# Kernel tuning notes

Measured on AMD Instinct MI355X. Metric: run time of the kernel, lower is better.

## Reference

```python
import jax, jax.numpy as jnp
import numpy as np

N_NODES = 32768
AGENTS = 32            # agents per sample (fully connected)
N_SAMPLES = N_NODES // AGENTS
N_EDGES = N_SAMPLES * AGENTS * (AGENTS - 1)  # 1,015,808
D = 64                 # latent_size
EDGE_DIM = 2
Z_DIM = 2 * D + EDGE_DIM  # CGConv concat width = 130
BN_EPS = 1e-5


def _build_block_edge_index():
    # fully-connected (no self-loop) blocks of AGENTS nodes, offset per sample
    a = np.arange(AGENTS)
    src, dst = np.meshgrid(a, a, indexing='ij')
    mask = src != dst
    src, dst = src[mask], dst[mask]              # [AGENTS*(AGENTS-1)]
    offs = (np.arange(N_SAMPLES) * AGENTS)[:, None]
    src = (src[None, :] + offs).reshape(-1)
    dst = (dst[None, :] + offs).reshape(-1)
    return jnp.asarray(np.stack([src, dst]), dtype=jnp.int64)


def setup_inputs() -> dict:
    key = jax.random.key(0)
    ks = jax.random.split(key, 16)
    x = jax.random.normal(ks[0], (N_NODES, D), dtype=jnp.float32)
    edge_index = _build_block_edge_index()                      # [2, E]
    edge_attr = jax.random.normal(ks[1], (N_EDGES, EDGE_DIM), dtype=jnp.float32)
    s = 1.0 / np.sqrt(Z_DIM)
    params = {}
    for li, base in ((1, 2), (2, 8)):
        params[f'Wf{li}'] = jax.random.uniform(ks[base + 0], (Z_DIM, D), jnp.float32, -s, s)
        params[f'bf{li}'] = jax.random.uniform(ks[base + 1], (D,), jnp.float32, -s, s)
        params[f'Ws{li}'] = jax.random.uniform(ks[base + 2], (Z_DIM, D), jnp.float32, -s, s)
        params[f'bs{li}'] = jax.random.uniform(ks[base + 3], (D,), jnp.float32, -s, s)
        params[f'gamma{li}'] = jnp.ones((D,), jnp.float32)
        params[f'beta{li}'] = jnp.zeros((D,), jnp.float32)
    return {'x': x, 'edge_index': edge_index, 'edge_attr': edge_attr, **params}


def _cgconv(x, edge_index, edge_attr, Wf, bf, Ws, bs, gamma, beta):
    src, dst = edge_index[0], edge_index[1]
    # z_ij = [x_i, x_j, e_ij], i = target (dst), j = source (src)
    z = jnp.concatenate([x[dst], x[src], edge_attr], axis=-1)       # [E, Z_DIM]
    m = jax.nn.sigmoid(z @ Wf + bf) * jax.nn.softplus(z @ Ws + bs)  # gated message
    agg = jax.ops.segment_sum(m, dst, num_segments=x.shape[0])      # scatter-add
    mu = jnp.mean(agg, axis=0)
    var = jnp.var(agg, axis=0)
    agg = (agg - mu) * jax.lax.rsqrt(var + BN_EPS) * gamma + beta   # train-mode BN
    return agg + x                                                  # residual


def reference(x, edge_index, edge_attr,
              Wf1, bf1, Ws1, bs1, gamma1, beta1,
              Wf2, bf2, Ws2, bs2, gamma2, beta2):
    h = jax.nn.relu(_cgconv(x, edge_index, edge_attr, Wf1, bf1, Ws1, bs1, gamma1, beta1))
    out = jax.nn.relu(_cgconv(h, edge_index, edge_attr, Wf2, bf2, Ws2, bs2, gamma2, beta2))
    return out
```

## Files before the change

kernel.cpp:

```cpp
#include <hip/hip_runtime.h>


#define NSAMP 1024
#define AG 32
#define DD 64
#define EPB 992
#define NN 32768
#define R1S 132

typedef float f4 __attribute__((ext_vector_type(4)));
typedef float f2 __attribute__((ext_vector_type(2)));

#define L2E 1.44269504088896340736f
#define BN_EPS_SCALED (1e-5 * (double)L2E * (double)L2E)

__device__ __forceinline__ void gacc(f4& acc, const f4 mf, const f4 ms) {
#pragma unroll
  for (int k = 0; k < 4; ++k) {
    float sig = __builtin_amdgcn_rcpf(1.0f + __builtin_amdgcn_exp2f(-mf[k]));
    float sp  = fmaxf(ms[k], 0.0f)
              + __builtin_amdgcn_logf(1.0f + __builtin_amdgcn_exp2f(-fabsf(ms[k])));
    acc[k] += sig * sp;
  }
}

template <int SRC>
__device__ __forceinline__ void gpass(const float* __restrict__ Wf,
                                      const float* __restrict__ bfv,
                                      const float* __restrict__ Ws,
                                      const float* __restrict__ bsv,
                                      const float* xb, float* R1,
                                      int t, int rbase) {
  const int tx = t & 31, ty = t >> 5;
  const int q = tx >> 4;
  const int cc0 = (tx & 15) * 4;
  const float* wbase = (q ? Ws : Wf) + SRC * (64 * 64) + cc0;
  constexpr int RPT = (SRC == 0) ? 2 : 4;
  f4 acc[RPT];
  if constexpr (SRC == 0) {
    const float* bv = q ? bsv : bfv;
    f4 b = *(const f4*)(bv + cc0);
#pragma unroll
    for (int r = 0; r < RPT; ++r) acc[r] = b;
  } else {
    f4 z = {0.f, 0.f, 0.f, 0.f};
#pragma unroll
    for (int r = 0; r < RPT; ++r) acc[r] = z;
  }
#pragma unroll 4
  for (int k4 = 0; k4 < 16; ++k4) {
    const float* wp = wbase + k4 * 256;
    f4 w0 = *(const f4*)(wp);
    f4 w1 = *(const f4*)(wp + 64);
    f4 w2 = *(const f4*)(wp + 128);
    f4 w3 = *(const f4*)(wp + 192);
#pragma unroll
    for (int r = 0; r < RPT; ++r) {
      const int row = (SRC == 0) ? (rbase + ty * RPT + r) : (ty * RPT + r);
      f4 xv = *(const f4*)&xb[row * 64 + k4 * 4];
      acc[r] += xv.x * w0 + xv.y * w1 + xv.z * w2 + xv.w * w3;
    }
  }
#pragma unroll
  for (int r = 0; r < RPT; ++r)
    *(f4*)&R1[(ty * RPT + r) * R1S + q * 64 + cc0] = acc[r] * L2E;
}

__device__ __forceinline__ void layer_body(
    int t, int s, int rbase, const float* __restrict__ ea,
    const float* __restrict__ Wf, const float* __restrict__ bfv,
    const float* __restrict__ Ws, const float* __restrict__ bsv,
    float* xb, float* R1, float* __restrict__ agg, double* __restrict__ stats)
{
  gpass<0>(Wf, bfv, Ws, bsv, xb, R1, t, rbase);
  __syncthreads();
  const int il = t >> 4, c0 = (t & 15) * 4;
  f4 af  = *(const f4*)&R1[il * R1S + c0];
  f4 as_ = *(const f4*)&R1[il * R1S + 64 + c0];
  __syncthreads();
  gpass<1>(Wf, bfv, Ws, bsv, xb, R1, t, 0);

  f4 wf0 = *(const f4*)(Wf + 128 * 64 + c0) * L2E;
  f4 wf1 = *(const f4*)(Wf + 129 * 64 + c0) * L2E;
  f4 ws0 = *(const f4*)(Ws + 128 * 64 + c0) * L2E;
  f4 ws1 = *(const f4*)(Ws + 129 * 64 + c0) * L2E;
  __syncthreads();

  {
    const f2* esrc = ((const f2*)ea) + (size_t)s * EPB;
    f2* ed = (f2*)xb;
    for (int u = t; u < EPB; u += 256) ed[u] = esrc[u];
  }
  __syncthreads();

  const int i = rbase + il;
  f4 acc = {0.f, 0.f, 0.f, 0.f};
  for (int jj = 0; jj < 31; ++jj) {
    const int ge = (jj >= i) ? 1 : 0;
    const int j  = jj + ge;
    const int e  = j * 31 + i - 1 + ge;
    f2 eav = *(const f2*)&xb[e * 2];
    f4 bf_ = *(const f4*)&R1[j * R1S + c0];
    f4 bs_ = *(const f4*)&R1[j * R1S + 64 + c0];
    f4 mf = af  + bf_ + eav.x * wf0 + eav.y * wf1;
    f4 ms = as_ + bs_ + eav.x * ws0 + eav.y * ws1;
    gacc(acc, mf, ms);
  }
  *(f4*)(agg + ((size_t)s * AG + i) * DD + c0) = acc;

  f4 s1 = acc, sq = acc * acc;
#pragma unroll
  for (int k = 0; k < 4; ++k) {
    s1[k] += __shfl_xor(s1[k], 16); sq[k] += __shfl_xor(sq[k], 16);
    s1[k] += __shfl_xor(s1[k], 32); sq[k] += __shfl_xor(sq[k], 32);
  }
  __syncthreads();
  if (t < 128) R1[t] = 0.0f;
  __syncthreads();
  if ((t & 63) < 16) {
#pragma unroll
    for (int k = 0; k < 4; ++k) {
      atomicAdd(&R1[c0 + k],      s1[k]);
      atomicAdd(&R1[64 + c0 + k], sq[k]);
    }
  }
  __syncthreads();
  if (t < 128) atomicAdd(&stats[t], (double)R1[t]);
}

__global__ __launch_bounds__(256, 4) void k_edge1(
    const float* __restrict__ x, const float* __restrict__ ea,
    const float* __restrict__ Wf, const float* __restrict__ bfv,
    const float* __restrict__ Ws, const float* __restrict__ bsv,
    float* __restrict__ agg, double* __restrict__ stats)
{
  __shared__ __align__(16) float xb[2048];
  __shared__ __align__(16) float R1[32 * R1S];
  const int t = threadIdx.x, b = blockIdx.x;
  const int s = b >> 1, rbase = (b & 1) * 16;
  {
    const f4* src = (const f4*)(x + (size_t)s * AG * DD);
    f4* dst = (f4*)xb;
    dst[t]       = src[t];
    dst[t + 256] = src[t + 256];
  }
  __syncthreads();
  layer_body(t, s, rbase, ea, Wf, bfv, Ws, bsv, xb, R1, agg, stats);
}

__global__ __launch_bounds__(256, 4) void k_edge2(
    const float* __restrict__ x, const float* __restrict__ ea,
    const float* __restrict__ Wf, const float* __restrict__ bfv,
    const float* __restrict__ Ws, const float* __restrict__ bsv,
    const double* __restrict__ stats1, const float* __restrict__ gmv,
    const float* __restrict__ btv, float* __restrict__ hout,
    const float* __restrict__ agg1, float* __restrict__ agg2,
    double* __restrict__ stats2)
{
  __shared__ __align__(16) float xb[2048];
  __shared__ __align__(16) float R1[32 * R1S];
  const int t = threadIdx.x, b = blockIdx.x;
  const int s = b >> 1, rbase = (b & 1) * 16;

  if (t < 64) {
    double mu  = stats1[t] * (1.0 / NN);
    double var = stats1[64 + t] * (1.0 / NN) - mu * mu;
    float rs = (float)(1.0 / sqrt(var + BN_EPS_SCALED));
    float g  = gmv[t] * rs;
    R1[t]      = g;
    R1[64 + t] = btv[t] - (float)mu * g;
  }
  __syncthreads();
  {
    const int row = t >> 3, cc = (t & 7) * 8;
    const size_t base = ((size_t)s * AG + row) * DD + cc;
    f4 sc0 = *(const f4*)&R1[cc],      sc1 = *(const f4*)&R1[cc + 4];
    f4 sh0 = *(const f4*)&R1[64 + cc], sh1 = *(const f4*)&R1[64 + cc + 4];
    f4 a0 = *(const f4*)(agg1 + base), a1 = *(const f4*)(agg1 + base + 4);
    f4 x0 = *(const f4*)(x + base),    x1 = *(const f4*)(x + base + 4);
    f4 h0 = a0 * sc0 + sh0 + x0;
    f4 h1 = a1 * sc1 + sh1 + x1;
#pragma unroll
    for (int k = 0; k < 4; ++k) { h0[k] = fmaxf(h0[k], 0.f); h1[k] = fmaxf(h1[k], 0.f); }
    *(f4*)(hout + base)     = h0;
    *(f4*)(hout + base + 4) = h1;
    *(f4*)&xb[row * DD + cc]     = h0;
    *(f4*)&xb[row * DD + cc + 4] = h1;
  }
  __syncthreads();
  layer_body(t, s, rbase, ea, Wf, bfv, Ws, bsv, xb, R1, agg2, stats2);
}

__global__ __launch_bounds__(256) void k_norm(
    const float* __restrict__ agg, const double* __restrict__ stats,
    const float* __restrict__ gmv, const float* __restrict__ btv,
    float* __restrict__ outp)
{
  __shared__ __align__(16) float sc[DD];
  __shared__ __align__(16) float sh[DD];
  const int t = threadIdx.x;
  if (t < DD) {
    double mu  = stats[t] * (1.0 / NN);
    double var = stats[DD + t] * (1.0 / NN) - mu * mu;
    float rs = (float)(1.0 / sqrt(var + BN_EPS_SCALED));
    float g  = gmv[t] * rs;
    sc[t] = g;
    sh[t] = btv[t] - (float)mu * g;
  }
  __syncthreads();
  const int idx = blockIdx.x * 256 + t;
  const int c   = (idx * 4) & (DD - 1);
  f4 a = ((const f4*)agg)[idx];
  f4 h = ((const f4*)outp)[idx];
  f4 r = a * (*(const f4*)&sc[c]) + (*(const f4*)&sh[c]) + h;
#pragma unroll
  for (int k = 0; k < 4; ++k) r[k] = fmaxf(r[k], 0.0f);
  ((f4*)outp)[idx] = r;
}

extern "C" void kernel_launch(void* const* d_in, const int* in_sizes, int n_in,
                              void* d_out, int out_size, void* d_ws, size_t ws_size,
                              hipStream_t stream) {
  const float* x   = (const float*)d_in[0];
  const float* ea  = (const float*)d_in[2];
  const float* Wf1 = (const float*)d_in[3];
  const float* bf1 = (const float*)d_in[4];
  const float* Ws1 = (const float*)d_in[5];
  const float* bs1 = (const float*)d_in[6];
  const float* gm1 = (const float*)d_in[7];
  const float* bt1 = (const float*)d_in[8];
  const float* Wf2 = (const float*)d_in[9];
  const float* bf2 = (const float*)d_in[10];
  const float* Ws2 = (const float*)d_in[11];
  const float* bs2 = (const float*)d_in[12];
  const float* gm2 = (const float*)d_in[13];
  const float* bt2 = (const float*)d_in[14];

  double* stats = (double*)d_ws;
  float*  agg1  = (float*)((char*)d_ws + 4096);
  float*  agg2  = (float*)((char*)d_ws + 4096 + (size_t)NN * DD * 4);
  float*  outp  = (float*)d_out;

  hipMemsetAsync(d_ws, 0, 2048, stream);
  k_edge1<<<2 * NSAMP, 256, 0, stream>>>(x, ea, Wf1, bf1, Ws1, bs1, agg1, stats);
  k_edge2<<<2 * NSAMP, 256, 0, stream>>>(x, ea, Wf2, bf2, Ws2, bs2,
                                         stats, gm1, bt1, outp, agg1, agg2,
                                         stats + 128);
  k_norm<<<NN * DD / 4 / 256, 256, 0, stream>>>(agg2, stats + 128, gm2, bt2, outp);
}
```

Before: 294.6 us.

## Process each sample in one 512-thread block to drop duplicated source projection

Each sample's 32 nodes are now handled by a single 512-thread block instead of two 256-thread blocks of 16 target rows each. Before, each half-block recomputed the full 32-row source-side projection, so that GEMM ran twice per sample; now it runs once. The two aggregation buffers are merged into one, with layer 2 reading its own sample's rows before overwriting them. The risk is that launch_bounds(512,4) lowers the per-thread register budget, which could cause spilling, and there are half as many blocks to spread across the GPU.

```diff
diff --git a/kernel.cpp b/kernel.cpp
--- a/kernel.cpp
+++ b/kernel.cpp
@@ -29,24 +29,21 @@
                                       const float* __restrict__ bfv,
                                       const float* __restrict__ Ws,
                                       const float* __restrict__ bsv,
-                                      const float* xb, float* R1,
-                                      int t, int rbase) {
+                                      const float* xb, float* R1, int t) {
   const int tx = t & 31, ty = t >> 5;
   const int q = tx >> 4;
   const int cc0 = (tx & 15) * 4;
   const float* wbase = (q ? Ws : Wf) + SRC * (64 * 64) + cc0;
-  constexpr int RPT = (SRC == 0) ? 2 : 4;
-  f4 acc[RPT];
+  f4 acc0, acc1;
   if constexpr (SRC == 0) {
     const float* bv = q ? bsv : bfv;
     f4 b = *(const f4*)(bv + cc0);
-#pragma unroll
-    for (int r = 0; r < RPT; ++r) acc[r] = b;
+    acc0 = b; acc1 = b;
   } else {
     f4 z = {0.f, 0.f, 0.f, 0.f};
-#pragma unroll
-    for (int r = 0; r < RPT; ++r) acc[r] = z;
-  }
+    acc0 = z; acc1 = z;
+  }
+  const int r0 = ty * 2;
 #pragma unroll 4
   for (int k4 = 0; k4 < 16; ++k4) {
     const float* wp = wbase + k4 * 256;
@@ -54,31 +51,28 @@
     f4 w1 = *(const f4*)(wp + 64);
     f4 w2 = *(const f4*)(wp + 128);
     f4 w3 = *(const f4*)(wp + 192);
-#pragma unroll
-    for (int r = 0; r < RPT; ++r) {
-      const int row = (SRC == 0) ? (rbase + ty * RPT + r) : (ty * RPT + r);
-      f4 xv = *(const f4*)&xb[row * 64 + k4 * 4];
-      acc[r] += xv.x * w0 + xv.y * w1 + xv.z * w2 + xv.w * w3;
-    }
-  }
-#pragma unroll
-  for (int r = 0; r < RPT; ++r)
-    *(f4*)&R1[(ty * RPT + r) * R1S + q * 64 + cc0] = acc[r] * L2E;
+    f4 xv0 = *(const f4*)&xb[r0 * 64 + k4 * 4];
+    f4 xv1 = *(const f4*)&xb[(r0 + 1) * 64 + k4 * 4];
+    acc0 += xv0.x * w0 + xv0.y * w1 + xv0.z * w2 + xv0.w * w3;
+    acc1 += xv1.x * w0 + xv1.y * w1 + xv1.z * w2 + xv1.w * w3;
+  }
+  *(f4*)&R1[r0 * R1S + q * 64 + cc0]       = acc0 * L2E;
+  *(f4*)&R1[(r0 + 1) * R1S + q * 64 + cc0] = acc1 * L2E;
 }
 
 __device__ __forceinline__ void layer_body(
-    int t, int s, int rbase, const float* __restrict__ ea,
+    int t, int s, const float* __restrict__ ea,
     const float* __restrict__ Wf, const float* __restrict__ bfv,
     const float* __restrict__ Ws, const float* __restrict__ bsv,
     float* xb, float* R1, float* __restrict__ agg, double* __restrict__ stats)
 {
-  gpass<0>(Wf, bfv, Ws, bsv, xb, R1, t, rbase);
-  __syncthreads();
-  const int il = t >> 4, c0 = (t & 15) * 4;
-  f4 af  = *(const f4*)&R1[il * R1S + c0];
-  f4 as_ = *(const f4*)&R1[il * R1S + 64 + c0];
-  __syncthreads();
-  gpass<1>(Wf, bfv, Ws, bsv, xb, R1, t, 0);
+  gpass<0>(Wf, bfv, Ws, bsv, xb, R1, t);
+  __syncthreads();
+  const int i = t >> 4, c0 = (t & 15) * 4;
+  f4 af  = *(const f4*)&R1[i * R1S + c0];
+  f4 as_ = *(const f4*)&R1[i * R1S + 64 + c0];
+  __syncthreads();
+  gpass<1>(Wf, bfv, Ws, bsv, xb, R1, t);
 
   f4 wf0 = *(const f4*)(Wf + 128 * 64 + c0) * L2E;
   f4 wf1 = *(const f4*)(Wf + 129 * 64 + c0) * L2E;
@@ -89,11 +83,10 @@
   {
     const f2* esrc = ((const f2*)ea) + (size_t)s * EPB;
     f2* ed = (f2*)xb;
-    for (int u = t; u < EPB; u += 256) ed[u] = esrc[u];
-  }
-  __syncthreads();
-
-  const int i = rbase + il;
+    for (int u = t; u < EPB; u += 512) ed[u] = esrc[u];
+  }
+  __syncthreads();
+
   f4 acc = {0.f, 0.f, 0.f, 0.f};
   for (int jj = 0; jj < 31; ++jj) {
     const int ge = (jj >= i) ? 1 : 0;
@@ -128,7 +121,7 @@
   if (t < 128) atomicAdd(&stats[t], (double)R1[t]);
 }
 
-__global__ __launch_bounds__(256, 4) void k_edge1(
+__global__ __launch_bounds__(512, 4) void k_edge1(
     const float* __restrict__ x, const float* __restrict__ ea,
     const float* __restrict__ Wf, const float* __restrict__ bfv,
     const float* __restrict__ Ws, const float* __restrict__ bsv,
@@ -136,31 +129,23 @@
 {
   __shared__ __align__(16) float xb[2048];
   __shared__ __align__(16) float R1[32 * R1S];
-  const int t = threadIdx.x, b = blockIdx.x;
-  const int s = b >> 1, rbase = (b & 1) * 16;
-  {
-    const f4* src = (const f4*)(x + (size_t)s * AG * DD);
-    f4* dst = (f4*)xb;
-    dst[t]       = src[t];
-    dst[t + 256] = src[t + 256];
-  }
-  __syncthreads();
-  layer_body(t, s, rbase, ea, Wf, bfv, Ws, bsv, xb, R1, agg, stats);
-}
-
-__global__ __launch_bounds__(256, 4) void k_edge2(
+  const int t = threadIdx.x, s = blockIdx.x;
+  ((f4*)xb)[t] = ((const f4*)(x + (size_t)s * AG * DD))[t];
+  __syncthreads();
+  layer_body(t, s, ea, Wf, bfv, Ws, bsv, xb, R1, agg, stats);
+}
+
+__global__ __launch_bounds__(512, 4) void k_edge2(
     const float* __restrict__ x, const float* __restrict__ ea,
     const float* __restrict__ Wf, const float* __restrict__ bfv,
     const float* __restrict__ Ws, const float* __restrict__ bsv,
     const double* __restrict__ stats1, const float* __restrict__ gmv,
     const float* __restrict__ btv, float* __restrict__ hout,
-    const float* __restrict__ agg1, float* __restrict__ agg2,
-    double* __restrict__ stats2)
+    float* __restrict__ agg, double* __restrict__ stats2)
 {
   __shared__ __align__(16) float xb[2048];
   __shared__ __align__(16) float R1[32 * R1S];
-  const int t = threadIdx.x, b = blockIdx.x;
-  const int s = b >> 1, rbase = (b & 1) * 16;
+  const int t = threadIdx.x, s = blockIdx.x;
 
   if (t < 64) {
     double mu  = stats1[t] * (1.0 / NN);
@@ -172,23 +157,18 @@
   }
   __syncthreads();
   {
-    const int row = t >> 3, cc = (t & 7) * 8;
+    const int row = t >> 4, cc = (t & 15) * 4;
     const size_t base = ((size_t)s * AG + row) * DD + cc;
-    f4 sc0 = *(const f4*)&R1[cc],      sc1 = *(const f4*)&R1[cc + 4];
-    f4 sh0 = *(const f4*)&R1[64 + cc], sh1 = *(const f4*)&R1[64 + cc + 4];
-    f4 a0 = *(const f4*)(agg1 + base), a1 = *(const f4*)(agg1 + base + 4);
-    f4 x0 = *(const f4*)(x + base),    x1 = *(const f4*)(x + base + 4);
-    f4 h0 = a0 * sc0 + sh0 + x0;
-    f4 h1 = a1 * sc1 + sh1 + x1;
-#pragma unroll
-    for (int k = 0; k < 4; ++k) { h0[k] = fmaxf(h0[k], 0.f); h1[k] = fmaxf(h1[k], 0.f); }
-    *(f4*)(hout + base)     = h0;
-    *(f4*)(hout + base + 4) = h1;
-    *(f4*)&xb[row * DD + cc]     = h0;
-    *(f4*)&xb[row * DD + cc + 4] = h1;
-  }
-  __syncthreads();
-  layer_body(t, s, rbase, ea, Wf, bfv, Ws, bsv, xb, R1, agg2, stats2);
+    f4 a  = *(const f4*)(agg + base);
+    f4 x0 = *(const f4*)(x + base);
+    f4 h = a * (*(const f4*)&R1[cc]) + (*(const f4*)&R1[64 + cc]) + x0;
+#pragma unroll
+    for (int k = 0; k < 4; ++k) h[k] = fmaxf(h[k], 0.f);
+    *(f4*)(hout + base) = h;
+    *(f4*)&xb[row * DD + cc] = h;
+  }
+  __syncthreads();
+  layer_body(t, s, ea, Wf, bfv, Ws, bsv, xb, R1, agg, stats2);
 }
 
 __global__ __launch_bounds__(256) void k_norm(
@@ -237,14 +217,12 @@
   const float* bt2 = (const float*)d_in[14];
 
   double* stats = (double*)d_ws;
-  float*  agg1  = (float*)((char*)d_ws + 4096);
-  float*  agg2  = (float*)((char*)d_ws + 4096 + (size_t)NN * DD * 4);
+  float*  agg   = (float*)((char*)d_ws + 4096);
   float*  outp  = (float*)d_out;
 
   hipMemsetAsync(d_ws, 0, 2048, stream);
-  k_edge1<<<2 * NSAMP, 256, 0, stream>>>(x, ea, Wf1, bf1, Ws1, bs1, agg1, stats);
-  k_edge2<<<2 * NSAMP, 256, 0, stream>>>(x, ea, Wf2, bf2, Ws2, bs2,
-                                         stats, gm1, bt1, outp, agg1, agg2,
-                                         stats + 128);
-  k_norm<<<NN * DD / 4 / 256, 256, 0, stream>>>(agg2, stats + 128, gm2, bt2, outp);
-}
+  k_edge1<<<NSAMP, 512, 0, stream>>>(x, ea, Wf1, bf1, Ws1, bs1, agg, stats);
+  k_edge2<<<NSAMP, 512, 0, stream>>>(x, ea, Wf2, bf2, Ws2, bs2,
+                                     stats, gm1, bt1, outp, agg, stats + 128);
+  k_norm<<<NN * DD / 4 / 256, 256, 0, stream>>>(agg, stats + 128, gm2, bt2, outp);
+}
```

Result: faster. 248.9 us (-15.5%).
